# Performance work log

Hardware: AMD Instinct MI355X
Metric: run time of the kernel (lower is better)

Reference implementation:

```python
import jax, jax.numpy as jnp
import numpy as np

B, N_ATOMS, N_ALIGN = 65536, 128, 64


def setup_inputs() -> dict:
    key = jax.random.key(0)
    k1, k2 = jax.random.split(key)
    traj = jax.random.normal(k1, (B, N_ATOMS, 3), dtype=jnp.float32)
    ref_pos = jax.random.normal(k2, (N_ATOMS, 3), dtype=jnp.float32)
    align_idx = jnp.arange(N_ALIGN, dtype=jnp.int32)  # 0-based (ids - 1)
    return {"traj": traj, "ref_pos": ref_pos, "align_idx": align_idx}


def reference(traj, ref_pos, align_idx):
    # --- __init__: centered reference coordinates of alignment atoms ---
    ref_x = ref_pos[align_idx]                      # [K, 3]
    ref_x = ref_x - jnp.mean(ref_x, axis=0)         # center

    # --- forward: Kabsch alignment per frame ---
    sel = traj[:, align_idx, :]                     # [B, K, 3]
    x_c = jnp.mean(sel, axis=1, keepdims=True)      # [B, 1, 3]
    x_notran = sel - x_c                            # [B, K, 3]
    # xtmp = x_notran^T  -> prod[b] = x_notran[b]^T @ ref_x : [B, 3, 3]
    prod = jnp.einsum('bki,kj->bij', x_notran, ref_x)

    u, s, vh = jnp.linalg.svd(prod)                 # u,vh: [B, 3, 3]
    sign_vec = jnp.sign(jnp.linalg.det(u @ vh))     # [B]
    # diag(1, 1, sign) applied on the right of u
    d = jnp.stack([jnp.ones_like(sign_vec), jnp.ones_like(sign_vec), sign_vec], axis=-1)
    rotate_mat = (u * d[:, None, :]) @ vh           # [B, 3, 3]

    aligned_traj = jnp.matmul(traj - x_c, rotate_mat)  # [B, N, 3]
    return aligned_traj
```

## Files before the change

kernel.cpp:

```cpp
#include <hip/hip_runtime.h>
#include <math.h>

#define NATOMS 128
#define NALIGN 64
#define WPB    8
#define FPW    2
#define FPB    (WPB * FPW)
#define TPB    (WPB * 64)

#define JACOBI_ROT(app, aqq, apq, arp, arq, pcol, qcol)                 \
  {                                                                     \
    float _apq = (apq);                                                 \
    float _den = 2.0f * _apq;                                           \
    _den = copysignf(fmaxf(fabsf(_den), 1e-30f), _den);                 \
    float _tau = ((aqq) - (app)) / _den;                                \
    float _t = (_tau >= 0.0f ? 1.0f : -1.0f) /                          \
               (fabsf(_tau) + sqrtf(1.0f + _tau * _tau));               \
    float _c = rsqrtf(1.0f + _t * _t);                                  \
    float _s = _t * _c;                                                 \
    (app) -= _t * _apq;                                                 \
    (aqq) += _t * _apq;                                                 \
    (apq) = 0.0f;                                                       \
    float _rp = (arp), _rq = (arq);                                     \
    (arp) = _c * _rp - _s * _rq;                                        \
    (arq) = _s * _rp + _c * _rq;                                        \
    _Pragma("unroll")                                                   \
    for (int _r = 0; _r < 3; _r++) {                                    \
      float _vp = v[3 * _r + (pcol)], _vq = v[3 * _r + (qcol)];         \
      v[3 * _r + (pcol)] = _c * _vp - _s * _vq;                         \
      v[3 * _r + (qcol)] = _s * _vp + _c * _vq;                         \
    }                                                                   \
  }

__device__ __forceinline__ void svd_rotation(const float* m, float* R)
{
    float a00 = m[0]*m[0] + m[3]*m[3] + m[6]*m[6];
    float a01 = m[0]*m[1] + m[3]*m[4] + m[6]*m[7];
    float a02 = m[0]*m[2] + m[3]*m[5] + m[6]*m[8];
    float a11 = m[1]*m[1] + m[4]*m[4] + m[7]*m[7];
    float a12 = m[1]*m[2] + m[4]*m[5] + m[7]*m[8];
    float a22 = m[2]*m[2] + m[5]*m[5] + m[8]*m[8];

    float v[9] = {1.f,0.f,0.f, 0.f,1.f,0.f, 0.f,0.f,1.f};
    #pragma unroll
    for (int sweep = 0; sweep < 5; sweep++) {
        JACOBI_ROT(a00, a11, a01, a02, a12, 0, 1);
        JACOBI_ROT(a00, a22, a02, a01, a12, 0, 2);
        JACOBI_ROT(a11, a22, a12, a01, a02, 1, 2);
    }

    float dd[3] = {a00, a11, a22};
    #pragma unroll
    for (int pass = 0; pass < 3; pass++) {
        const int ii = (pass == 2) ? 1 : 0;
        const int jj = (pass == 0) ? 1 : 2;
        float di = dd[ii], dj = dd[jj];
        bool sw = di < dj;
        dd[ii] = sw ? dj : di;
        dd[jj] = sw ? di : dj;
        #pragma unroll
        for (int rr = 0; rr < 3; rr++) {
            float a = v[3*rr+ii], b = v[3*rr+jj];
            v[3*rr+ii] = sw ? b : a;
            v[3*rr+jj] = sw ? a : b;
        }
    }

    float v0x = v[0], v0y = v[3], v0z = v[6];
    float v1x = v[1], v1y = v[4], v1z = v[7];
    float v2x = v[2], v2y = v[5], v2z = v[8];

    float u1x = m[0]*v0x + m[1]*v0y + m[2]*v0z;
    float u1y = m[3]*v0x + m[4]*v0y + m[5]*v0z;
    float u1z = m[6]*v0x + m[7]*v0y + m[8]*v0z;
    float n1 = rsqrtf(fmaxf(u1x*u1x + u1y*u1y + u1z*u1z, 1e-30f));
    u1x *= n1; u1y *= n1; u1z *= n1;

    float u2x = m[0]*v1x + m[1]*v1y + m[2]*v1z;
    float u2y = m[3]*v1x + m[4]*v1y + m[5]*v1z;
    float u2z = m[6]*v1x + m[7]*v1y + m[8]*v1z;
    float d12 = u1x*u2x + u1y*u2y + u1z*u2z;
    u2x -= d12 * u1x; u2y -= d12 * u1y; u2z -= d12 * u1z;
    float n2 = rsqrtf(fmaxf(u2x*u2x + u2y*u2y + u2z*u2z, 1e-30f));
    u2x *= n2; u2y *= n2; u2z *= n2;

    float u3x = u1y*u2z - u1z*u2y;
    float u3y = u1z*u2x - u1x*u2z;
    float u3z = u1x*u2y - u1y*u2x;
    float cxv = v1y*v2z - v1z*v2y;
    float cyv = v1z*v2x - v1x*v2z;
    float czv = v1x*v2y - v1y*v2x;
    float detv = v0x*cxv + v0y*cyv + v0z*czv;
    float sg = (detv >= 0.f) ? 1.f : -1.f;
    u3x *= sg; u3y *= sg; u3z *= sg;

    R[0] = u1x*v0x + u2x*v1x + u3x*v2x;
    R[1] = u1x*v0y + u2x*v1y + u3x*v2y;
    R[2] = u1x*v0z + u2x*v1z + u3x*v2z;
    R[3] = u1y*v0x + u2y*v1x + u3y*v2x;
    R[4] = u1y*v0y + u2y*v1y + u3y*v2y;
    R[5] = u1y*v0z + u2y*v1z + u3y*v2z;
    R[6] = u1z*v0x + u2z*v1x + u3z*v2x;
    R[7] = u1z*v0y + u2z*v1y + u3z*v2y;
    R[8] = u1z*v0z + u2z*v1z + u3z*v2z;
}

__device__ __forceinline__ int slotAddr(int o, int so) {
    return (o << 6) | ((so << 4) ^ ((o & 6) << 3));
}

__global__ __launch_bounds__(TPB) void align_kernel(
    const float* __restrict__ traj,
    const float* __restrict__ ref_pos,
    const int* __restrict__ align_idx,
    float* __restrict__ out,
    int B)
{
    __shared__ float4 s_rmap[NATOMS];
    __shared__ __align__(16) float s_stage[WPB][1024];
    __shared__ float s_cov[FPB][13];

    const int t = threadIdx.x;
    const int w = t >> 6;
    const int l = t & 63;
    const int chunk0 = blockIdx.x * FPB + w * FPW;
    const int lim = B * 96;

    const float4* __restrict__ gin = (const float4*)traj;
    char* wst = (char*)&s_stage[w][0];

    float4 st[3];
    #pragma unroll
    for (int c = 0; c < 3; c++) {
        int gq = chunk0 * 96 + c * 64 + l;
        st[c] = (gq < lim) ? gin[gq] : make_float4(0.f, 0.f, 0.f, 0.f);
    }

    if (t < NALIGN) {
        const float4 z4 = make_float4(0.f, 0.f, 0.f, 0.f);
        s_rmap[t]          = z4;
        s_rmap[t + NALIGN] = z4;
        int idx = align_idx[t];
        float rx = ref_pos[idx * 3 + 0];
        float ry = ref_pos[idx * 3 + 1];
        float rz = ref_pos[idx * 3 + 2];
        float sx = rx, sy = ry, sz = rz;
        #pragma unroll
        for (int off = 32; off >= 1; off >>= 1) {
            sx += __shfl_xor(sx, off);
            sy += __shfl_xor(sy, off);
            sz += __shfl_xor(sz, off);
        }
        const float inv = 1.0f / (float)NALIGN;
        int slot = ((idx & 3) << 5) | (idx >> 2);
        s_rmap[slot] = make_float4(rx - sx*inv, ry - sy*inv, rz - sz*inv, 1.0f);
    }

    #pragma unroll
    for (int c = 0; c < 3; c++) {
        int q  = c * 64 + l;
        int o  = q / 3;
        int so = q - 3 * o;
        *(float4*)(wst + slotAddr(o, so)) = st[c];
    }
    __syncthreads();

    float4 u0 = *(const float4*)(wst + slotAddr(l, 0));
    float4 u1 = *(const float4*)(wst + slotAddr(l, 1));
    float4 u2 = *(const float4*)(wst + slotAddr(l, 2));
    float x[4] = { u0.x, u0.w, u1.z, u2.y };
    float y[4] = { u0.y, u1.x, u1.w, u2.z };
    float z[4] = { u0.z, u1.y, u2.x, u2.w };

    const int lf = l & 31;
    {
        float sx = 0.f, sy = 0.f, sz = 0.f;
        float c9[9] = {0.f,0.f,0.f,0.f,0.f,0.f,0.f,0.f,0.f};
        #pragma unroll
        for (int j = 0; j < 4; j++) {
            float4 rm = s_rmap[(j << 5) | lf];
            sx += rm.w * x[j]; sy += rm.w * y[j]; sz += rm.w * z[j];
            c9[0] += x[j]*rm.x; c9[1] += x[j]*rm.y; c9[2] += x[j]*rm.z;
            c9[3] += y[j]*rm.x; c9[4] += y[j]*rm.y; c9[5] += y[j]*rm.z;
            c9[6] += z[j]*rm.x; c9[7] += z[j]*rm.y; c9[8] += z[j]*rm.z;
        }
        #pragma unroll
        for (int off = 16; off >= 1; off >>= 1) {
            sx += __shfl_xor(sx, off);
            sy += __shfl_xor(sy, off);
            sz += __shfl_xor(sz, off);
            #pragma unroll
            for (int jj = 0; jj < 9; jj++) c9[jj] += __shfl_xor(c9[jj], off);
        }
        if (lf == 0) {
            int fi = w * FPW + (l >> 5);
            #pragma unroll
            for (int jj = 0; jj < 9; jj++) s_cov[fi][jj] = c9[jj];
            const float inv = 1.0f / (float)NALIGN;
            s_cov[fi][9]  = sx * inv;
            s_cov[fi][10] = sy * inv;
            s_cov[fi][11] = sz * inv;
        }
    }
    __syncthreads();

    if (t < FPB && (blockIdx.x * FPB + t) < B) {
        float m[9];
        #pragma unroll
        for (int j = 0; j < 9; j++) m[j] = s_cov[t][j];
        float R[9];
        svd_rotation(m, R);
        #pragma unroll
        for (int j = 0; j < 9; j++) s_cov[t][j] = R[j];
    }
    __syncthreads();

    {
        const int fi = w * FPW + (l >> 5);
        float R0 = s_cov[fi][0], R1 = s_cov[fi][1], R2 = s_cov[fi][2];
        float R3 = s_cov[fi][3], R4 = s_cov[fi][4], R5 = s_cov[fi][5];
        float R6 = s_cov[fi][6], R7 = s_cov[fi][7], R8 = s_cov[fi][8];
        float xcx = s_cov[fi][9], xcy = s_cov[fi][10], xcz = s_cov[fi][11];

        float ox[4], oy[4], oz[4];
        #pragma unroll
        for (int j = 0; j < 4; j++) {
            float dx = x[j] - xcx, dy = y[j] - xcy, dz = z[j] - xcz;
            ox[j] = dx*R0 + dy*R3 + dz*R6;
            oy[j] = dx*R1 + dy*R4 + dz*R7;
            oz[j] = dx*R2 + dy*R5 + dz*R8;
        }

        *(float4*)(wst + slotAddr(l, 0)) = make_float4(ox[0], oy[0], oz[0], ox[1]);
        *(float4*)(wst + slotAddr(l, 1)) = make_float4(oy[1], oz[1], ox[2], oy[2]);
        *(float4*)(wst + slotAddr(l, 2)) = make_float4(oz[2], ox[3], oy[3], oz[3]);
    }
    __syncthreads();

    float4* __restrict__ gout = (float4*)out;
    #pragma unroll
    for (int c = 0; c < 3; c++) {
        int q  = c * 64 + l;
        int o  = q / 3;
        int so = q - 3 * o;
        float4 v4 = *(const float4*)(wst + slotAddr(o, so));
        int gq = chunk0 * 96 + q;
        if (gq < lim) gout[gq] = v4;
    }
}

extern "C" void kernel_launch(void* const* d_in, const int* in_sizes, int n_in,
                              void* d_out, int out_size, void* d_ws, size_t ws_size,
                              hipStream_t stream) {
    const float* traj      = (const float*)d_in[0];
    const float* ref_pos   = (const float*)d_in[1];
    const int*   align_idx = (const int*)d_in[2];
    float*       out       = (float*)d_out;

    int B = in_sizes[0] / (NATOMS * 3);
    int grid = (B + FPB - 1) / FPB;
    align_kernel<<<grid, TPB, 0, stream>>>(traj, ref_pos, align_idx, out, B);
}
```

Before: 195.3 us.

## Restructure kernel into single-wave blocks processing 32 frames with prefetch pipeline

The kernel now uses 64-thread blocks, each handling 32 frames as 16 sequential tiles. A 4-deep register prefetch of global loads replaces block-wide __syncthreads with wave-local LDS fences. Covariances are computed in a first pass, then 32 lanes run the SVDs in parallel instead of 16 threads out of 512. A second pass re-reads traj from global memory to apply the rotations. This removes block barriers and idle SVD threads and improves latency hiding, at the cost of reading the input twice and running fewer waves per block.

Measured after the change: 245.2 us. 25.6% more time.

```diff
diff --git a/kernel.cpp b/kernel.cpp
--- a/kernel.cpp
+++ b/kernel.cpp
@@ -3,10 +3,13 @@
 
 #define NATOMS 128
 #define NALIGN 64
-#define WPB    8
-#define FPW    2
-#define FPB    (WPB * FPW)
-#define TPB    (WPB * 64)
+#define TPB    64
+#define FRW    32
+#define TILES  (FRW / 2)
+#define PF     4
+
+#define LDS_FENCE() do { asm volatile("s_waitcnt lgkmcnt(0)" ::: "memory"); \
+                         __builtin_amdgcn_sched_barrier(0); } while (0)
 
 #define JACOBI_ROT(app, aqq, apq, arp, arq, pcol, qcol)                 \
   {                                                                     \
@@ -117,30 +120,22 @@
     int B)
 {
     __shared__ float4 s_rmap[NATOMS];
-    __shared__ __align__(16) float s_stage[WPB][1024];
-    __shared__ float s_cov[FPB][13];
-
-    const int t = threadIdx.x;
-    const int w = t >> 6;
-    const int l = t & 63;
-    const int chunk0 = blockIdx.x * FPB + w * FPW;
-    const int lim = B * 96;
-
-    const float4* __restrict__ gin = (const float4*)traj;
-    char* wst = (char*)&s_stage[w][0];
-
-    float4 st[3];
-    #pragma unroll
-    for (int c = 0; c < 3; c++) {
-        int gq = chunk0 * 96 + c * 64 + l;
-        st[c] = (gq < lim) ? gin[gq] : make_float4(0.f, 0.f, 0.f, 0.f);
-    }
-
-    if (t < NALIGN) {
-        const float4 z4 = make_float4(0.f, 0.f, 0.f, 0.f);
-        s_rmap[t]          = z4;
-        s_rmap[t + NALIGN] = z4;
-        int idx = align_idx[t];
+    __shared__ __align__(16) char  s_stage[4096];
+    __shared__ __align__(16) float s_cov[FRW][20];
+
+    const int l    = threadIdx.x;
+    const int lf   = l & 31;
+    const int half = l >> 5;
+    const int q0   = blockIdx.x * (FRW * 96);
+    const int lim  = B * 96;
+    const float4 z4 = make_float4(0.f, 0.f, 0.f, 0.f);
+    const float4* __restrict__ gin  = (const float4*)traj;
+    float4* __restrict__       gout = (float4*)out;
+
+    {
+        s_rmap[l]          = z4;
+        s_rmap[l + NALIGN] = z4;
+        int idx = align_idx[l];
         float rx = ref_pos[idx * 3 + 0];
         float ry = ref_pos[idx * 3 + 1];
         float rz = ref_pos[idx * 3 + 2];
@@ -156,96 +151,164 @@
         s_rmap[slot] = make_float4(rx - sx*inv, ry - sy*inv, rz - sz*inv, 1.0f);
     }
 
+    float4 st[PF][3];
     #pragma unroll
-    for (int c = 0; c < 3; c++) {
-        int q  = c * 64 + l;
-        int o  = q / 3;
-        int so = q - 3 * o;
-        *(float4*)(wst + slotAddr(o, so)) = st[c];
-    }
-    __syncthreads();
-
-    float4 u0 = *(const float4*)(wst + slotAddr(l, 0));
-    float4 u1 = *(const float4*)(wst + slotAddr(l, 1));
-    float4 u2 = *(const float4*)(wst + slotAddr(l, 2));
-    float x[4] = { u0.x, u0.w, u1.z, u2.y };
-    float y[4] = { u0.y, u1.x, u1.w, u2.z };
-    float z[4] = { u0.z, u1.y, u2.x, u2.w };
-
-    const int lf = l & 31;
+    for (int p = 0; p < PF; p++)
+        #pragma unroll
+        for (int c = 0; c < 3; c++) {
+            int gq = q0 + (p * 3 + c) * 64 + l;
+            st[p][c] = (gq < lim) ? gin[gq] : z4;
+        }
+
+    #pragma unroll 1
+    for (int tb = 0; tb < TILES; tb += PF) {
+        #pragma unroll
+        for (int p = 0; p < PF; p++) {
+            const int t = tb + p;
+            #pragma unroll
+            for (int c = 0; c < 3; c++) {
+                int q  = c * 64 + l;
+                int o  = q / 3, so = q - 3 * o;
+                *(float4*)(s_stage + slotAddr(o, so)) = st[p][c];
+            }
+            LDS_FENCE();
+            float4 u0 = *(const float4*)(s_stage + slotAddr(l, 0));
+            float4 u1 = *(const float4*)(s_stage + slotAddr(l, 1));
+            float4 u2 = *(const float4*)(s_stage + slotAddr(l, 2));
+            LDS_FENCE();
+            float x[4] = { u0.x, u0.w, u1.z, u2.y };
+            float y[4] = { u0.y, u1.x, u1.w, u2.z };
+            float z[4] = { u0.z, u1.y, u2.x, u2.w };
+
+            float sx = 0.f, sy = 0.f, sz = 0.f;
+            float c9[9] = {0.f,0.f,0.f,0.f,0.f,0.f,0.f,0.f,0.f};
+            #pragma unroll
+            for (int j = 0; j < 4; j++) {
+                float4 rm = s_rmap[(j << 5) | lf];
+                sx += rm.w * x[j]; sy += rm.w * y[j]; sz += rm.w * z[j];
+                c9[0] += x[j]*rm.x; c9[1] += x[j]*rm.y; c9[2] += x[j]*rm.z;
+                c9[3] += y[j]*rm.x; c9[4] += y[j]*rm.y; c9[5] += y[j]*rm.z;
+                c9[6] += z[j]*rm.x; c9[7] += z[j]*rm.y; c9[8] += z[j]*rm.z;
+            }
+            #pragma unroll
+            for (int off = 16; off >= 1; off >>= 1) {
+                sx += __shfl_xor(sx, off);
+                sy += __shfl_xor(sy, off);
+                sz += __shfl_xor(sz, off);
+                #pragma unroll
+                for (int jj = 0; jj < 9; jj++) c9[jj] += __shfl_xor(c9[jj], off);
+            }
+            if (lf == 0) {
+                int fr = 2 * t + half;
+                const float inv = 1.0f / (float)NALIGN;
+                *(float4*)&s_cov[fr][0] = make_float4(c9[0], c9[1], c9[2], c9[3]);
+                *(float4*)&s_cov[fr][4] = make_float4(c9[4], c9[5], c9[6], c9[7]);
+                *(float4*)&s_cov[fr][8] = make_float4(c9[8], sx*inv, sy*inv, sz*inv);
+            }
+            if (t + PF < TILES) {
+                #pragma unroll
+                for (int c = 0; c < 3; c++) {
+                    int gq = q0 + ((t + PF) * 3 + c) * 64 + l;
+                    st[p][c] = (gq < lim) ? gin[gq] : z4;
+                }
+            }
+        }
+    }
+
+    LDS_FENCE();
     {
-        float sx = 0.f, sy = 0.f, sz = 0.f;
-        float c9[9] = {0.f,0.f,0.f,0.f,0.f,0.f,0.f,0.f,0.f};
-        #pragma unroll
-        for (int j = 0; j < 4; j++) {
-            float4 rm = s_rmap[(j << 5) | lf];
-            sx += rm.w * x[j]; sy += rm.w * y[j]; sz += rm.w * z[j];
-            c9[0] += x[j]*rm.x; c9[1] += x[j]*rm.y; c9[2] += x[j]*rm.z;
-            c9[3] += y[j]*rm.x; c9[4] += y[j]*rm.y; c9[5] += y[j]*rm.z;
-            c9[6] += z[j]*rm.x; c9[7] += z[j]*rm.y; c9[8] += z[j]*rm.z;
-        }
-        #pragma unroll
-        for (int off = 16; off >= 1; off >>= 1) {
-            sx += __shfl_xor(sx, off);
-            sy += __shfl_xor(sy, off);
-            sz += __shfl_xor(sz, off);
-            #pragma unroll
-            for (int jj = 0; jj < 9; jj++) c9[jj] += __shfl_xor(c9[jj], off);
-        }
-        if (lf == 0) {
-            int fi = w * FPW + (l >> 5);
-            #pragma unroll
-            for (int jj = 0; jj < 9; jj++) s_cov[fi][jj] = c9[jj];
-            const float inv = 1.0f / (float)NALIGN;
-            s_cov[fi][9]  = sx * inv;
-            s_cov[fi][10] = sy * inv;
-            s_cov[fi][11] = sz * inv;
-        }
-    }
-    __syncthreads();
-
-    if (t < FPB && (blockIdx.x * FPB + t) < B) {
-        float m[9];
-        #pragma unroll
-        for (int j = 0; j < 9; j++) m[j] = s_cov[t][j];
+        int fr = lf;
+        float4 a0 = *(const float4*)&s_cov[fr][0];
+        float4 a1 = *(const float4*)&s_cov[fr][4];
+        float4 a2 = *(const float4*)&s_cov[fr][8];
+        float m[9] = { a0.x, a0.y, a0.z, a0.w, a1.x, a1.y, a1.z, a1.w, a2.x };
         float R[9];
         svd_rotation(m, R);
-        #pragma unroll
-        for (int j = 0; j < 9; j++) s_cov[t][j] = R[j];
-    }
-    __syncthreads();
-
-    {
-        const int fi = w * FPW + (l >> 5);
-        float R0 = s_cov[fi][0], R1 = s_cov[fi][1], R2 = s_cov[fi][2];
-        float R3 = s_cov[fi][3], R4 = s_cov[fi][4], R5 = s_cov[fi][5];
-        float R6 = s_cov[fi][6], R7 = s_cov[fi][7], R8 = s_cov[fi][8];
-        float xcx = s_cov[fi][9], xcy = s_cov[fi][10], xcz = s_cov[fi][11];
-
-        float ox[4], oy[4], oz[4];
-        #pragma unroll
-        for (int j = 0; j < 4; j++) {
-            float dx = x[j] - xcx, dy = y[j] - xcy, dz = z[j] - xcz;
-            ox[j] = dx*R0 + dy*R3 + dz*R6;
-            oy[j] = dx*R1 + dy*R4 + dz*R7;
-            oz[j] = dx*R2 + dy*R5 + dz*R8;
-        }
-
-        *(float4*)(wst + slotAddr(l, 0)) = make_float4(ox[0], oy[0], oz[0], ox[1]);
-        *(float4*)(wst + slotAddr(l, 1)) = make_float4(oy[1], oz[1], ox[2], oy[2]);
-        *(float4*)(wst + slotAddr(l, 2)) = make_float4(oz[2], ox[3], oy[3], oz[3]);
-    }
-    __syncthreads();
-
-    float4* __restrict__ gout = (float4*)out;
+        LDS_FENCE();
+        if (l < 32) {
+            *(float4*)&s_cov[fr][0] = make_float4(R[0], R[1], R[2], R[3]);
+            *(float4*)&s_cov[fr][4] = make_float4(R[4], R[5], R[6], R[7]);
+            *(float4*)&s_cov[fr][8] = make_float4(R[8], a2.y, a2.z, a2.w);
+        }
+    }
+    LDS_FENCE();
+
     #pragma unroll
-    for (int c = 0; c < 3; c++) {
-        int q  = c * 64 + l;
-        int o  = q / 3;
-        int so = q - 3 * o;
-        float4 v4 = *(const float4*)(wst + slotAddr(o, so));
-        int gq = chunk0 * 96 + q;
-        if (gq < lim) gout[gq] = v4;
+    for (int p = 0; p < PF; p++)
+        #pragma unroll
+        for (int c = 0; c < 3; c++) {
+            int gq = q0 + (p * 3 + c) * 64 + l;
+            st[p][c] = (gq < lim) ? gin[gq] : z4;
+        }
+
+    #pragma unroll 1
+    for (int tb = 0; tb < TILES; tb += PF) {
+        #pragma unroll
+        for (int p = 0; p < PF; p++) {
+            const int t = tb + p;
+            #pragma unroll
+            for (int c = 0; c < 3; c++) {
+                int q  = c * 64 + l;
+                int o  = q / 3, so = q - 3 * o;
+                *(float4*)(s_stage + slotAddr(o, so)) = st[p][c];
+            }
+            LDS_FENCE();
+            float4 u0 = *(const float4*)(s_stage + slotAddr(l, 0));
+            float4 u1 = *(const float4*)(s_stage + slotAddr(l, 1));
+            float4 u2 = *(const float4*)(s_stage + slotAddr(l, 2));
+            LDS_FENCE();
+            float x[4] = { u0.x, u0.w, u1.z, u2.y };
+            float y[4] = { u0.y, u1.x, u1.w, u2.z };
+            float z[4] = { u0.z, u1.y, u2.x, u2.w };
+
+            int fr = 2 * t + half;
+            float4 a0 = *(const float4*)&s_cov[fr][0];
+            float4 a1 = *(const float4*)&s_cov[fr][4];
+            float4 a2 = *(const float4*)&s_cov[fr][8];
+            float R0 = a0.x, R1 = a0.y, R2 = a0.z, R3 = a0.w;
+            float R4 = a1.x, R5 = a1.y, R6 = a1.z, R7 = a1.w;
+            float R8 = a2.x, xcx = a2.y, xcy = a2.z, xcz = a2.w;
+
+            float ox[4], oy[4], oz[4];
+            #pragma unroll
+            for (int j = 0; j < 4; j++) {
+                float dx = x[j] - xcx, dy = y[j] - xcy, dz = z[j] - xcz;
+                ox[j] = dx*R0 + dy*R3 + dz*R6;
+                oy[j] = dx*R1 + dy*R4 + dz*R7;
+                oz[j] = dx*R2 + dy*R5 + dz*R8;
+            }
+
+            *(float4*)(s_stage + slotAddr(l, 0)) = make_float4(ox[0], oy[0], oz[0], ox[1]);
+            *(float4*)(s_stage + slotAddr(l, 1)) = make_float4(oy[1], oz[1], ox[2], oy[2]);
+            *(float4*)(s_stage + slotAddr(l, 2)) = make_float4(oz[2], ox[3], oy[3], oz[3]);
+            LDS_FENCE();
+            float4 v0, v1, v2;
+            {
+                int q, o, so;
+                q = 0 * 64 + l; o = q / 3; so = q - 3 * o;
+                v0 = *(const float4*)(s_stage + slotAddr(o, so));
+                q = 1 * 64 + l; o = q / 3; so = q - 3 * o;
+                v1 = *(const float4*)(s_stage + slotAddr(o, so));
+                q = 2 * 64 + l; o = q / 3; so = q - 3 * o;
+                v2 = *(const float4*)(s_stage + slotAddr(o, so));
+            }
+            LDS_FENCE();
+            {
+                int gq0 = q0 + (t * 3 + 0) * 64 + l;
+                int gq1 = q0 + (t * 3 + 1) * 64 + l;
+                int gq2 = q0 + (t * 3 + 2) * 64 + l;
+                if (gq0 < lim) gout[gq0] = v0;
+                if (gq1 < lim) gout[gq1] = v1;
+                if (gq2 < lim) gout[gq2] = v2;
+            }
+            if (t + PF < TILES) {
+                #pragma unroll
+                for (int c = 0; c < 3; c++) {
+                    int gq = q0 + ((t + PF) * 3 + c) * 64 + l;
+                    st[p][c] = (gq < lim) ? gin[gq] : z4;
+                }
+            }
+        }
     }
 }
 
@@ -258,6 +321,6 @@
     float*       out       = (float*)d_out;
 
     int B = in_sizes[0] / (NATOMS * 3);
-    int grid = (B + FPB - 1) / FPB;
+    int grid = (B + FRW - 1) / FRW;
     align_kernel<<<grid, TPB, 0, stream>>>(traj, ref_pos, align_idx, out, B);
 }
```
